# Optimization experiments

Hardware: AMD Instinct MI355X
Metric: run time of the kernel (lower is better)

The kernel has to match this reference:

```python
import jax, jax.numpy as jnp
import numpy as np

B, DIM, H, W = 16, 256, 64, 64
HEADS, DHEAD, MEM = 4, 32, 4
HIDDEN = HEADS * DHEAD


def setup_inputs() -> dict:
    key = jax.random.key(0)
    ks = jax.random.split(key, 4)
    return {
        "x": jax.random.normal(ks[0], (B, DIM, H, W), dtype=jnp.float32),
        "g1": jnp.ones((DIM,), dtype=jnp.float32),
        "w_qkv": jax.random.normal(ks[1], (3 * HIDDEN, DIM), dtype=jnp.float32) * 0.02,
        "mem_kv": jax.random.normal(ks[2], (2, HEADS, DHEAD, MEM), dtype=jnp.float32),
        "w_out": jax.random.normal(ks[3], (DIM, HIDDEN), dtype=jnp.float32) * 0.02,
        "b_out": jnp.zeros((DIM,), dtype=jnp.float32),
        "g2": jnp.ones((DIM,), dtype=jnp.float32),
    }


def _rmsnorm(x, g):
    # F.normalize(x, dim=1) * g * sqrt(dim); g broadcast over (1, dim, 1, 1)
    n = jnp.sqrt(jnp.sum(x * x, axis=1, keepdims=True))
    scale = jnp.asarray(x.shape[1], x.dtype) ** 0.5
    return x / jnp.maximum(n, 1e-12) * g[None, :, None, None] * scale


def reference(x, g1, w_qkv, mem_kv, w_out, b_out, g2):
    b, c, h, w = x.shape
    attn_scale = DHEAD ** -0.5
    xn = _rmsnorm(x, g1)
    # 1x1 conv == channel matmul; chunk(3, dim=1) -> leading axis 3 after reshape
    qkv = jnp.einsum('oc,bchw->bohw', w_qkv, xn)
    qkv = qkv.reshape(b, 3, HEADS, DHEAD, h * w)  # b 3 h d n
    q, k, v = qkv[:, 0], qkv[:, 1], qkv[:, 2]
    mk = jnp.broadcast_to(mem_kv[0][None], (b, HEADS, DHEAD, MEM))
    mv = jnp.broadcast_to(mem_kv[1][None], (b, HEADS, DHEAD, MEM))
    k = jnp.concatenate([mk, k], axis=-1)  # b h d (m+n)
    v = jnp.concatenate([mv, v], axis=-1)
    q = jax.nn.softmax(q, axis=-2) * attn_scale  # softmax over feature dim d
    k = jax.nn.softmax(k, axis=-1)               # softmax over token dim n
    context = jnp.einsum('bhdn,bhen->bhde', k, v)  # d x e per head
    out = jnp.einsum('bhde,bhdn->bhen', context, q)
    out = out.reshape(b, HIDDEN, h, w)
    out = jnp.einsum('oc,bchw->bohw', w_out, out) + b_out[None, :, None, None]
    return _rmsnorm(out, g2)
```

## Files before the change

kernel.cpp:

```cpp
#include <hip/hip_runtime.h>
#include <hip/hip_bf16.h>

#define NB 16
#define DIM 256
#define HW 4096
#define HEADS 4
#define DHEAD 32
#define MEM 4
#define HIDDEN 128

typedef __hip_bfloat16 bf16;
typedef __attribute__((ext_vector_type(8))) short bf16x8;
typedef __attribute__((ext_vector_type(4))) float f32x4;
typedef __attribute__((ext_vector_type(4))) unsigned short us4;

#define AS1 __attribute__((address_space(1)))
#define AS3 __attribute__((address_space(3)))

__device__ __forceinline__ void gld_lds16(const void* g, void* l) {
    __builtin_amdgcn_global_load_lds((const AS1 void*)g, (AS3 void*)l, 16, 0, 0);
}
__device__ __forceinline__ float b2f(short s) {
    union { unsigned int u; float f; } x; x.u = ((unsigned int)(unsigned short)s) << 16; return x.f;
}
__device__ __forceinline__ short f2bs(float f) {
    bf16 h = __float2bfloat16(f);
    return *reinterpret_cast<short*>(&h);
}

constexpr size_t OFF_W1B  = 0;
constexpr size_t OFF_RP   = OFF_W1B + 98304*2;
constexpr size_t OFF_PCTX = OFF_RP + 4*65536*4;
constexpr size_t OFF_CTXN = OFF_PCTX + (size_t)32*64*1056*4;
constexpr size_t OFF_M    = OFF_CTXN + (size_t)64*1024*4;
constexpr size_t OFF_QT   = OFF_M + (size_t)NB*DIM*HIDDEN*2;
constexpr size_t OFF_XT   = OFF_QT + (size_t)NB*HW*HIDDEN*2;

__global__ void k_prep(const float* __restrict__ wqkv, const float* __restrict__ g1,
                       short* __restrict__ w1b) {
    int i = blockIdx.x * 256 + threadIdx.x;
    w1b[i] = f2bs(wqkv[i] * g1[i & (DIM - 1)]);
}

__global__ __launch_bounds__(256) void k_tr(const float* __restrict__ x,
                                            short* __restrict__ xT,
                                            float* __restrict__ rpart) {
    int n0 = blockIdx.x * 64, cy = blockIdx.y, b = blockIdx.z;
    int c0 = cy * 64;
    __shared__ short xs[64 * 65];
    __shared__ float ps[4][64];
    int t = threadIdx.x;
    int ln = t & 63, cb = t >> 6;
    const float* xp = x + ((size_t)b * DIM + c0) * HW + n0;
    float ss = 0.f;
#pragma unroll
    for (int j = 0; j < 16; ++j) {
        int c = cb * 16 + j;
        float v = xp[(size_t)c * HW + ln];
        ss += v * v;
        xs[c * 65 + ln] = f2bs(v);
    }
    ps[cb][ln] = ss;
    __syncthreads();
    if (t < 64)
        rpart[((size_t)cy * NB + b) * HW + n0 + t] = ps[0][t] + ps[1][t] + ps[2][t] + ps[3][t];
    int n = t >> 2, ch = t & 3;
    alignas(16) short tmp[16];
#pragma unroll
    for (int i = 0; i < 16; ++i) tmp[i] = xs[(ch * 16 + i) * 65 + n];
    short* o = xT + ((size_t)b * HW + n0 + n) * DIM + c0 + ch * 16;
    *(bf16x8*)(o)     = *(bf16x8*)(tmp);
    *(bf16x8*)(o + 8) = *(bf16x8*)(tmp + 8);
}

__global__ __launch_bounds__(768) void k_gemm(const short* __restrict__ w1b,
                                              const short* __restrict__ xT,
                                              const float* __restrict__ rpart,
                                              short* __restrict__ qT,
                                              float* __restrict__ pctx) {
    __shared__ __align__(16) char smem[66048];
    float* r2s = (float*)(smem + 65536);
    int nt = blockIdx.x, b = blockIdx.y;
    int t = threadIdx.x;
    int w = t >> 6, lane = t & 63;
    int wr = w >> 1, wc = w & 1;
    int lr = lane & 15, lg = lane >> 4;
    const f32x4 fz = {0.f, 0.f, 0.f, 0.f};
    f32x4 acc[4][4];
#pragma unroll
    for (int m = 0; m < 4; ++m)
#pragma unroll
        for (int n = 0; n < 4; ++n) acc[m][n] = fz;

    if (t < 128) {
        int col = nt * 128 + t;
        float s = rpart[(size_t)b * HW + col] + rpart[(size_t)(16 + b) * HW + col]
                + rpart[(size_t)(32 + b) * HW + col] + rpart[(size_t)(48 + b) * HW + col];
        r2s[t] = 16.0f / fmaxf(sqrtf(s), 1e-12f);
    }

    const short* Bg = xT + ((size_t)b * HW + nt * 128) * 256;
#pragma unroll
    for (int is = 0; is < 5; ++is) {
        int o = is * 12288 + t * 16;
        int row = o >> 9;
        int js = ((o >> 4) & 31) ^ (row & 31);
        gld_lds16(Bg + (size_t)row * 256 + js * 8, smem + o);
    }
    if (t < 256) {
        int o = 61440 + t * 16;
        int row = o >> 9;
        int js = ((o >> 4) & 31) ^ (row & 31);
        gld_lds16(Bg + (size_t)row * 256 + js * 8, smem + o);
    }
    __syncthreads();

    const short* Ag = w1b + (size_t)(wr * 64 + lr) * 256 + lg * 8;
#pragma unroll 2
    for (int kt = 0; kt < 8; ++kt) {
        int kk = kt * 32;
        bf16x8 av[4], bv[4];
#pragma unroll
        for (int m = 0; m < 4; ++m)
            av[m] = *(const bf16x8*)(Ag + (size_t)m * 16 * 256 + kk);
#pragma unroll
        for (int nf = 0; nf < 4; ++nf) {
            int row = wc * 64 + nf * 16 + lr;
            int phys = (kt * 4 + lg) ^ (row & 31);
            bv[nf] = *(const bf16x8*)(smem + row * 512 + phys * 16);
        }
#pragma unroll
        for (int m = 0; m < 4; ++m)
#pragma unroll
            for (int nf = 0; nf < 4; ++nf)
                acc[m][nf] = __builtin_amdgcn_mfma_f32_16x16x32_bf16(av[m], bv[nf], acc[m][nf], 0, 0, 0);
    }

    int gcol0 = nt * 128 + wc * 64 + lr;
    float rv[4];
#pragma unroll
    for (int nf = 0; nf < 4; ++nf) rv[nf] = r2s[wc * 64 + nf * 16 + lr];

    __syncthreads();
    short* ekb = (short*)smem;
    short* vb  = (short*)(smem + 32768);

    if (wr < 2) {
#pragma unroll
        for (int nf = 0; nf < 4; ++nf) {
            int gcol = gcol0 + nf * 16;
#pragma unroll
            for (int a = 0; a < 2; ++a) {
                float v[8];
#pragma unroll
                for (int mm = 0; mm < 2; ++mm)
#pragma unroll
                    for (int q = 0; q < 4; ++q)
                        v[mm * 4 + q] = acc[2 * a + mm][nf][q] * rv[nf];
                float mx = v[0];
#pragma unroll
                for (int i = 1; i < 8; ++i) mx = fmaxf(mx, v[i]);
                mx = fmaxf(mx, __shfl_xor(mx, 16));
                mx = fmaxf(mx, __shfl_xor(mx, 32));
                float sum = 0.f;
#pragma unroll
                for (int i = 0; i < 8; ++i) { v[i] = __expf(v[i] - mx); sum += v[i]; }
                sum += __shfl_xor(sum, 16);
                sum += __shfl_xor(sum, 32);
                float inv = 0.17677669529663689f / sum;
                size_t base = ((size_t)b * HW + gcol) * 128 + (wr * 2 + a) * 32 + lg * 4;
#pragma unroll
                for (int mm = 0; mm < 2; ++mm) {
                    us4 pk;
#pragma unroll
                    for (int q = 0; q < 4; ++q)
                        pk[q] = (unsigned short)f2bs(v[mm * 4 + q] * inv);
                    *(us4*)(qT + base + mm * 16) = pk;
                }
            }
        }
    } else if (wr < 4) {
#pragma unroll
        for (int m = 0; m < 4; ++m)
#pragma unroll
            for (int nf = 0; nf < 4; ++nf)
#pragma unroll
                for (int q = 0; q < 4; ++q) {
                    int rloc = (wr - 2) * 64 + m * 16 + lg * 4 + q;
                    int col = wc * 64 + nf * 16 + lr;
                    int cs = ((((col >> 3) ^ (rloc & 15)) << 3) | (col & 7));
                    ekb[rloc * 128 + cs] = f2bs(__expf(acc[m][nf][q] * rv[nf]));
                }
    } else {
#pragma unroll
        for (int m = 0; m < 4; ++m)
#pragma unroll
            for (int nf = 0; nf < 4; ++nf)
#pragma unroll
                for (int q = 0; q < 4; ++q) {
                    int rloc = (wr - 4) * 64 + m * 16 + lg * 4 + q;
                    int col = wc * 64 + nf * 16 + lr;
                    int cs = ((((col >> 3) ^ (rloc & 15)) << 3) | (col & 7));
                    vb[rloc * 128 + cs] = f2bs(acc[m][nf][q] * rv[nf]);
                }
    }
    __syncthreads();
    if (w < 4) {
        int h = w;
        f32x4 c2[2][2];
        c2[0][0] = fz; c2[0][1] = fz; c2[1][0] = fz; c2[1][1] = fz;
#pragma unroll
        for (int ks = 0; ks < 4; ++ks) {
            int j = ks * 4 + lg;
            bf16x8 a2[2], b2[2];
#pragma unroll
            for (int mm = 0; mm < 2; ++mm) {
                int row = h * 32 + mm * 16 + lr;
                a2[mm] = *(const bf16x8*)(ekb + row * 128 + ((j ^ (row & 15)) << 3));
            }
#pragma unroll
            for (int nn = 0; nn < 2; ++nn) {
                int row = h * 32 + nn * 16 + lr;
                b2[nn] = *(const bf16x8*)(vb + row * 128 + ((j ^ (row & 15)) << 3));
            }
#pragma unroll
            for (int mm = 0; mm < 2; ++mm)
#pragma unroll
                for (int nn = 0; nn < 2; ++nn)
                    c2[mm][nn] = __builtin_amdgcn_mfma_f32_16x16x32_bf16(a2[mm], b2[nn], c2[mm][nn], 0, 0, 0);
        }
        float* o = pctx + ((size_t)nt * 64 + b * 4 + h) * 1056;
#pragma unroll
        for (int mm = 0; mm < 2; ++mm)
#pragma unroll
            for (int nn = 0; nn < 2; ++nn)
#pragma unroll
                for (int qq = 0; qq < 4; ++qq) {
                    int d = mm * 16 + lg * 4 + qq;
                    int e = nn * 16 + lr;
                    o[d * 32 + e] = c2[mm][nn][qq];
                }
    } else if (w >= 8) {
        int hd = (w - 8) * 32 + (lane & 31);
        int half = lane >> 5;
        float rs = 0.f;
#pragma unroll
        for (int blk = 0; blk < 8; ++blk) {
            int chunk = half * 8 + blk;
            bf16x8 e8 = *(const bf16x8*)(ekb + hd * 128 + ((chunk ^ (hd & 15)) << 3));
#pragma unroll
            for (int jj = 0; jj < 8; ++jj) rs += b2f(e8[jj]);
        }
        rs += __shfl_xor(rs, 32);
        if (lane < 32)
            pctx[((size_t)nt * 64 + b * 4 + (w - 8)) * 1056 + 1024 + (lane & 31)] = rs;
    }
}

__global__ __launch_bounds__(256) void k_red(const float* __restrict__ pctx,
                                             const float* __restrict__ memkv,
                                             float* __restrict__ ctxn) {
    int ds = blockIdx.x, bh = blockIdx.y;
    int t = threadIdx.x;
    int dd = t >> 5, ee = t & 31;
    int d = ds * 8 + dd;
    int h = bh & 3;
    __shared__ float rss[8];
    float s = 0.f;
#pragma unroll 8
    for (int c = 0; c < 32; ++c)
        s += pctx[((size_t)c * 64 + bh) * 1056 + d * 32 + ee];
    if (t < 8) {
        int d2 = ds * 8 + t;
        float rs = 0.f;
#pragma unroll 8
        for (int c = 0; c < 32; ++c)
            rs += pctx[((size_t)c * 64 + bh) * 1056 + 1024 + d2];
#pragma unroll
        for (int m2 = 0; m2 < MEM; ++m2) rs += __expf(memkv[(h * 32 + d2) * MEM + m2]);
        rss[t] = rs;
    }
    float mem = 0.f;
#pragma unroll
    for (int m2 = 0; m2 < MEM; ++m2)
        mem += __expf(memkv[(h * 32 + d) * MEM + m2]) * memkv[512 + (h * 32 + ee) * MEM + m2];
    __syncthreads();
    ctxn[(size_t)bh * 1024 + d * 32 + ee] = (s + mem) / rss[dd];
}

__global__ __launch_bounds__(256) void k_M2(const float* __restrict__ ctxn,
                                            const float* __restrict__ wout,
                                            short* __restrict__ Mmat) {
    int og = blockIdx.x, b = blockIdx.y;
    __shared__ float ctx[4 * 33 * 33];
    __shared__ float wsw[32 * 136];
    int t = threadIdx.x;
#pragma unroll
    for (int j = 0; j < 16; ++j) {
        int e = t + j * 256;
        int h = e >> 10, dd = (e >> 5) & 31, ee = e & 31;
        ctx[h * 1089 + dd * 33 + ee] = ctxn[(size_t)(b * 4 + h) * 1024 + (e & 1023)];
    }
#pragma unroll
    for (int j = 0; j < 4; ++j) {
        int e4 = t + j * 256;
        int row = e4 >> 5, c = (e4 & 31) * 4;
        f32x4 w4 = *(const f32x4*)(wout + (size_t)(og * 32 + row) * HIDDEN + c);
        *(f32x4*)(wsw + row * 136 + (c >> 5) * 34 + (c & 31)) = w4;
    }
    __syncthreads();
    int ol = t >> 3, hg = t & 7;
    alignas(16) short out16[16];
#pragma unroll
    for (int ii = 0; ii < 16; ++ii) {
        int hd = hg * 16 + ii;
        int h = hd >> 5, dd = hd & 31;
        float s = 0.f;
#pragma unroll
        for (int e = 0; e < 32; ++e)
            s += wsw[ol * 136 + h * 34 + e] * ctx[h * 1089 + dd * 33 + e];
        out16[ii] = f2bs(s);
    }
    short* op = Mmat + ((size_t)(b * 256 + og * 32 + ol)) * 128 + hg * 16;
    *(bf16x8*)(op)     = *(bf16x8*)(out16);
    *(bf16x8*)(op + 8) = *(bf16x8*)(out16 + 8);
}

__global__ __launch_bounds__(256) void k_out2(const short* __restrict__ Mmat,
                                              const short* __restrict__ qT,
                                              const float* __restrict__ bout,
                                              const float* __restrict__ g2,
                                              float* __restrict__ out) {
    int nt = blockIdx.x, b = blockIdx.y;
    __shared__ short As[256 * 64];
    __shared__ short Bs[64 * 64];
    __shared__ float sw[4][80];
    __shared__ float r2s[64];
    int t = threadIdx.x;
    int wave = t >> 6, lane = t & 63;
    int lr = lane & 15, lg = lane >> 4;
    const short* Ag = Mmat + (size_t)b * 256 * 128;
    const short* Bg = qT + ((size_t)b * HW + nt * 64) * 128;
    const f32x4 fz = {0.f, 0.f, 0.f, 0.f};
    f32x4 acc[4][4];
#pragma unroll
    for (int m = 0; m < 4; ++m)
#pragma unroll
        for (int n = 0; n < 4; ++n) acc[m][n] = fz;

    for (int kk = 0; kk < 128; kk += 64) {
        if (kk) __syncthreads();
#pragma unroll
        for (int is = 0; is < 8; ++is) {
            int o = is * 4096 + t * 16;
            int rr2 = o >> 7;
            int js = ((o >> 4) & 7) ^ (rr2 & 7);
            gld_lds16(Ag + (size_t)rr2 * 128 + kk + js * 8, (char*)As + o);
        }
#pragma unroll
        for (int is = 0; is < 2; ++is) {
            int o = is * 4096 + t * 16;
            int rr2 = o >> 7;
            int js = ((o >> 4) & 7) ^ (rr2 & 7);
            gld_lds16(Bg + (size_t)rr2 * 128 + kk + js * 8, (char*)Bs + o);
        }
        __syncthreads();
#pragma unroll
        for (int ks = 0; ks < 2; ++ks) {
            bf16x8 av[4], bv[4];
            int j = lg + 4 * ks;
#pragma unroll
            for (int m = 0; m < 4; ++m) {
                int row = wave * 64 + m * 16 + lr;
                av[m] = *(const bf16x8*)((const char*)As + row * 128 + ((j ^ (row & 7)) << 4));
            }
#pragma unroll
            for (int n = 0; n < 4; ++n) {
                int row = n * 16 + lr;
                bv[n] = *(const bf16x8*)((const char*)Bs + row * 128 + ((j ^ (row & 7)) << 4));
            }
#pragma unroll
            for (int m = 0; m < 4; ++m)
#pragma unroll
                for (int n = 0; n < 4; ++n)
                    acc[m][n] = __builtin_amdgcn_mfma_f32_16x16x32_bf16(av[m], bv[n], acc[m][n], 0, 0, 0);
        }
    }
    float bb[4][4], gg[4][4];
#pragma unroll
    for (int m = 0; m < 4; ++m)
#pragma unroll
        for (int q = 0; q < 4; ++q) {
            int row = wave * 64 + m * 16 + lg * 4 + q;
            bb[m][q] = bout[row];
            gg[m][q] = g2[row];
        }
    float ssn[4] = {0.f, 0.f, 0.f, 0.f};
#pragma unroll
    for (int n = 0; n < 4; ++n)
#pragma unroll
        for (int m = 0; m < 4; ++m)
#pragma unroll
            for (int q = 0; q < 4; ++q) {
                float val = acc[m][n][q] + bb[m][q];
                acc[m][n][q] = val;
                ssn[n] += val * val;
            }
#pragma unroll
    for (int n = 0; n < 4; ++n) {
        ssn[n] += __shfl_xor(ssn[n], 16);
        ssn[n] += __shfl_xor(ssn[n], 32);
    }
    if (lg == 0) {
#pragma unroll
        for (int n = 0; n < 4; ++n) sw[wave][n * 16 + lr] = ssn[n];
    }
    __syncthreads();
    if (t < 64) {
        float s = sw[0][t] + sw[1][t] + sw[2][t] + sw[3][t];
        r2s[t] = 16.0f / fmaxf(sqrtf(s), 1e-12f);
    }
    __syncthreads();
    float* op = out + (size_t)b * DIM * HW + nt * 64;
#pragma unroll
    for (int n = 0; n < 4; ++n) {
        float rc = r2s[n * 16 + lr];
#pragma unroll
        for (int m = 0; m < 4; ++m)
#pragma unroll
            for (int q = 0; q < 4; ++q) {
                int row = wave * 64 + m * 16 + lg * 4 + q;
                op[(size_t)row * HW + n * 16 + lr] = acc[m][n][q] * rc * gg[m][q];
            }
    }
}

extern "C" void kernel_launch(void* const* d_in, const int* in_sizes, int n_in,
                              void* d_out, int out_size, void* d_ws, size_t ws_size,
                              hipStream_t stream) {
    const float* x     = (const float*)d_in[0];
    const float* g1    = (const float*)d_in[1];
    const float* wqkv  = (const float*)d_in[2];
    const float* memkv = (const float*)d_in[3];
    const float* wout  = (const float*)d_in[4];
    const float* bout  = (const float*)d_in[5];
    const float* g2    = (const float*)d_in[6];
    float* out = (float*)d_out;
    char* ws = (char*)d_ws;

    short* w1b  = (short*)(ws + OFF_W1B);
    float* rpart= (float*)(ws + OFF_RP);
    float* pctx = (float*)(ws + OFF_PCTX);
    float* ctxn = (float*)(ws + OFF_CTXN);
    short* Mmat = (short*)(ws + OFF_M);
    short* qT   = (short*)(ws + OFF_QT);
    short* xT   = (short*)(ws + OFF_XT);

    k_prep<<<384, 256, 0, stream>>>(wqkv, g1, w1b);
    k_tr<<<dim3(64, 4, NB), 256, 0, stream>>>(x, xT, rpart);
    k_gemm<<<dim3(32, NB), 768, 0, stream>>>(w1b, xT, rpart, qT, pctx);
    k_red<<<dim3(4, 64), 256, 0, stream>>>(pctx, memkv, ctxn);
    k_M2<<<dim3(8, NB), 256, 0, stream>>>(ctxn, wout, Mmat);
    k_out2<<<dim3(64, NB), 256, 0, stream>>>(Mmat, qT, bout, g2, out);
}
```

Measured before the change: 91.56 us.

## Halve QKV GEMM token tile to 64 with 384-thread blocks and register A prefetch

The fused QKV projection and context kernel now processes 64 tokens per block with 6 waves instead of 128 tokens with 12 waves. That doubles the grid to 1024 blocks and halves LDS use so up to three blocks can reside per CU. Each wave holds its full 64-row weight slice in registers, loaded in two halves, rather than reloading per k-step. The softmax-K and V staging in LDS drops the XOR swizzle. The partial-context buffer and the reduction kernel double to 64 chunks, which adds reduction traffic and raises register pressure.

```diff
diff --git a/kernel.cpp b/kernel.cpp
--- a/kernel.cpp
+++ b/kernel.cpp
@@ -31,7 +31,7 @@
 constexpr size_t OFF_W1B  = 0;
 constexpr size_t OFF_RP   = OFF_W1B + 98304*2;
 constexpr size_t OFF_PCTX = OFF_RP + 4*65536*4;
-constexpr size_t OFF_CTXN = OFF_PCTX + (size_t)32*64*1056*4;
+constexpr size_t OFF_CTXN = OFF_PCTX + (size_t)64*64*1056*4;
 constexpr size_t OFF_M    = OFF_CTXN + (size_t)64*1024*4;
 constexpr size_t OFF_QT   = OFF_M + (size_t)NB*DIM*HIDDEN*2;
 constexpr size_t OFF_XT   = OFF_QT + (size_t)NB*HW*HIDDEN*2;
@@ -73,17 +73,17 @@
     *(bf16x8*)(o + 8) = *(bf16x8*)(tmp + 8);
 }
 
-__global__ __launch_bounds__(768) void k_gemm(const short* __restrict__ w1b,
-                                              const short* __restrict__ xT,
-                                              const float* __restrict__ rpart,
-                                              short* __restrict__ qT,
-                                              float* __restrict__ pctx) {
-    __shared__ __align__(16) char smem[66048];
-    float* r2s = (float*)(smem + 65536);
+__global__ __launch_bounds__(384, 3) void k_gemm(const short* __restrict__ w1b,
+                                                 const short* __restrict__ xT,
+                                                 const float* __restrict__ rpart,
+                                                 short* __restrict__ qT,
+                                                 float* __restrict__ pctx) {
+    __shared__ __align__(16) char smem[33280];
+    float* r2s = (float*)(smem + 32768);
     int nt = blockIdx.x, b = blockIdx.y;
+    int n0g = nt * 64;
     int t = threadIdx.x;
     int w = t >> 6, lane = t & 63;
-    int wr = w >> 1, wc = w & 1;
     int lr = lane & 15, lg = lane >> 4;
     const f32x4 fz = {0.f, 0.f, 0.f, 0.f};
     f32x4 acc[4][4];
@@ -92,63 +92,84 @@
 #pragma unroll
         for (int n = 0; n < 4; ++n) acc[m][n] = fz;
 
+    const short* Bg = xT + ((size_t)b * HW + n0g) * 256;
+#pragma unroll
+    for (int is = 0; is < 5; ++is) {
+        int o = is * 6144 + t * 16;
+        int row = o >> 9;
+        int js = ((o >> 4) & 31) ^ (row & 31);
+        gld_lds16(Bg + (size_t)row * 256 + js * 8, smem + o);
+    }
     if (t < 128) {
-        int col = nt * 128 + t;
+        int o = 30720 + t * 16;
+        int row = o >> 9;
+        int js = ((o >> 4) & 31) ^ (row & 31);
+        gld_lds16(Bg + (size_t)row * 256 + js * 8, smem + o);
+    }
+    if (t < 64) {
+        int col = n0g + t;
         float s = rpart[(size_t)b * HW + col] + rpart[(size_t)(16 + b) * HW + col]
                 + rpart[(size_t)(32 + b) * HW + col] + rpart[(size_t)(48 + b) * HW + col];
         r2s[t] = 16.0f / fmaxf(sqrtf(s), 1e-12f);
     }
-
-    const short* Bg = xT + ((size_t)b * HW + nt * 128) * 256;
-#pragma unroll
-    for (int is = 0; is < 5; ++is) {
-        int o = is * 12288 + t * 16;
-        int row = o >> 9;
-        int js = ((o >> 4) & 31) ^ (row & 31);
-        gld_lds16(Bg + (size_t)row * 256 + js * 8, smem + o);
-    }
-    if (t < 256) {
-        int o = 61440 + t * 16;
-        int row = o >> 9;
-        int js = ((o >> 4) & 31) ^ (row & 31);
-        gld_lds16(Bg + (size_t)row * 256 + js * 8, smem + o);
-    }
-    __syncthreads();
-
-    const short* Ag = w1b + (size_t)(wr * 64 + lr) * 256 + lg * 8;
-#pragma unroll 2
-    for (int kt = 0; kt < 8; ++kt) {
-        int kk = kt * 32;
-        bf16x8 av[4], bv[4];
-#pragma unroll
-        for (int m = 0; m < 4; ++m)
-            av[m] = *(const bf16x8*)(Ag + (size_t)m * 16 * 256 + kk);
+    const short* Ag = w1b + (size_t)(w * 64 + lr) * 256 + lg * 8;
+    bf16x8 a1[4][4];
+#pragma unroll
+    for (int m = 0; m < 4; ++m)
+#pragma unroll
+        for (int kc = 0; kc < 4; ++kc)
+            a1[m][kc] = *(const bf16x8*)(Ag + (size_t)m * 16 * 256 + kc * 32);
+    __syncthreads();
+
+#pragma unroll
+    for (int kc = 0; kc < 4; ++kc) {
+        bf16x8 bv[4];
 #pragma unroll
         for (int nf = 0; nf < 4; ++nf) {
-            int row = wc * 64 + nf * 16 + lr;
-            int phys = (kt * 4 + lg) ^ (row & 31);
+            int row = nf * 16 + lr;
+            int phys = (kc * 4 + lg) ^ (row & 31);
             bv[nf] = *(const bf16x8*)(smem + row * 512 + phys * 16);
         }
 #pragma unroll
         for (int m = 0; m < 4; ++m)
 #pragma unroll
             for (int nf = 0; nf < 4; ++nf)
-                acc[m][nf] = __builtin_amdgcn_mfma_f32_16x16x32_bf16(av[m], bv[nf], acc[m][nf], 0, 0, 0);
-    }
-
-    int gcol0 = nt * 128 + wc * 64 + lr;
+                acc[m][nf] = __builtin_amdgcn_mfma_f32_16x16x32_bf16(a1[m][kc], bv[nf], acc[m][nf], 0, 0, 0);
+    }
+    bf16x8 a2[4][4];
+#pragma unroll
+    for (int m = 0; m < 4; ++m)
+#pragma unroll
+        for (int kc = 0; kc < 4; ++kc)
+            a2[m][kc] = *(const bf16x8*)(Ag + (size_t)m * 16 * 256 + 128 + kc * 32);
+#pragma unroll
+    for (int kc = 0; kc < 4; ++kc) {
+        bf16x8 bv[4];
+#pragma unroll
+        for (int nf = 0; nf < 4; ++nf) {
+            int row = nf * 16 + lr;
+            int phys = ((kc + 4) * 4 + lg) ^ (row & 31);
+            bv[nf] = *(const bf16x8*)(smem + row * 512 + phys * 16);
+        }
+#pragma unroll
+        for (int m = 0; m < 4; ++m)
+#pragma unroll
+            for (int nf = 0; nf < 4; ++nf)
+                acc[m][nf] = __builtin_amdgcn_mfma_f32_16x16x32_bf16(a2[m][kc], bv[nf], acc[m][nf], 0, 0, 0);
+    }
+
     float rv[4];
 #pragma unroll
-    for (int nf = 0; nf < 4; ++nf) rv[nf] = r2s[wc * 64 + nf * 16 + lr];
+    for (int nf = 0; nf < 4; ++nf) rv[nf] = r2s[nf * 16 + lr];
 
     __syncthreads();
     short* ekb = (short*)smem;
-    short* vb  = (short*)(smem + 32768);
-
-    if (wr < 2) {
+    short* vb  = (short*)(smem + 16384);
+
+    if (w < 2) {
 #pragma unroll
         for (int nf = 0; nf < 4; ++nf) {
-            int gcol = gcol0 + nf * 16;
+            int gcol = n0g + nf * 16 + lr;
 #pragma unroll
             for (int a = 0; a < 2; ++a) {
                 float v[8];
@@ -168,7 +189,7 @@
                 sum += __shfl_xor(sum, 16);
                 sum += __shfl_xor(sum, 32);
                 float inv = 0.17677669529663689f / sum;
-                size_t base = ((size_t)b * HW + gcol) * 128 + (wr * 2 + a) * 32 + lg * 4;
+                size_t base = ((size_t)b * HW + gcol) * 128 + (w * 2 + a) * 32 + lg * 4;
 #pragma unroll
                 for (int mm = 0; mm < 2; ++mm) {
                     us4 pk;
@@ -179,17 +200,15 @@
                 }
             }
         }
-    } else if (wr < 4) {
+    } else if (w < 4) {
 #pragma unroll
         for (int m = 0; m < 4; ++m)
 #pragma unroll
             for (int nf = 0; nf < 4; ++nf)
 #pragma unroll
                 for (int q = 0; q < 4; ++q) {
-                    int rloc = (wr - 2) * 64 + m * 16 + lg * 4 + q;
-                    int col = wc * 64 + nf * 16 + lr;
-                    int cs = ((((col >> 3) ^ (rloc & 15)) << 3) | (col & 7));
-                    ekb[rloc * 128 + cs] = f2bs(__expf(acc[m][nf][q] * rv[nf]));
+                    int rloc = (w - 2) * 64 + m * 16 + lg * 4 + q;
+                    ekb[rloc * 64 + nf * 16 + lr] = f2bs(__expf(acc[m][nf][q] * rv[nf]));
                 }
     } else {
 #pragma unroll
@@ -198,10 +217,8 @@
             for (int nf = 0; nf < 4; ++nf)
 #pragma unroll
                 for (int q = 0; q < 4; ++q) {
-                    int rloc = (wr - 4) * 64 + m * 16 + lg * 4 + q;
-                    int col = wc * 64 + nf * 16 + lr;
-                    int cs = ((((col >> 3) ^ (rloc & 15)) << 3) | (col & 7));
-                    vb[rloc * 128 + cs] = f2bs(acc[m][nf][q] * rv[nf]);
+                    int rloc = (w - 4) * 64 + m * 16 + lg * 4 + q;
+                    vb[rloc * 64 + nf * 16 + lr] = f2bs(acc[m][nf][q] * rv[nf]);
                 }
     }
     __syncthreads();
@@ -210,24 +227,20 @@
         f32x4 c2[2][2];
         c2[0][0] = fz; c2[0][1] = fz; c2[1][0] = fz; c2[1][1] = fz;
 #pragma unroll
-        for (int ks = 0; ks < 4; ++ks) {
-            int j = ks * 4 + lg;
-            bf16x8 a2[2], b2[2];
-#pragma unroll
-            for (int mm = 0; mm < 2; ++mm) {
-                int row = h * 32 + mm * 16 + lr;
-                a2[mm] = *(const bf16x8*)(ekb + row * 128 + ((j ^ (row & 15)) << 3));
-            }
-#pragma unroll
-            for (int nn = 0; nn < 2; ++nn) {
-                int row = h * 32 + nn * 16 + lr;
-                b2[nn] = *(const bf16x8*)(vb + row * 128 + ((j ^ (row & 15)) << 3));
-            }
+        for (int ks = 0; ks < 2; ++ks) {
+            int j = lg + 4 * ks;
+            bf16x8 a2b[2], b2[2];
 #pragma unroll
             for (int mm = 0; mm < 2; ++mm)
+                a2b[mm] = *(const bf16x8*)(ekb + (h * 32 + mm * 16 + lr) * 64 + j * 8);
+#pragma unroll
+            for (int nn = 0; nn < 2; ++nn)
+                b2[nn] = *(const bf16x8*)(vb + (h * 32 + nn * 16 + lr) * 64 + j * 8);
+#pragma unroll
+            for (int mm = 0; mm < 2; ++mm)
 #pragma unroll
                 for (int nn = 0; nn < 2; ++nn)
-                    c2[mm][nn] = __builtin_amdgcn_mfma_f32_16x16x32_bf16(a2[mm], b2[nn], c2[mm][nn], 0, 0, 0);
+                    c2[mm][nn] = __builtin_amdgcn_mfma_f32_16x16x32_bf16(a2b[mm], b2[nn], c2[mm][nn], 0, 0, 0);
         }
         float* o = pctx + ((size_t)nt * 64 + b * 4 + h) * 1056;
 #pragma unroll
@@ -240,20 +253,16 @@
                     int e = nn * 16 + lr;
                     o[d * 32 + e] = c2[mm][nn][qq];
                 }
-    } else if (w >= 8) {
-        int hd = (w - 8) * 32 + (lane & 31);
-        int half = lane >> 5;
+    } else {
+        int hd = (w - 4) * 64 + lane;
         float rs = 0.f;
 #pragma unroll
         for (int blk = 0; blk < 8; ++blk) {
-            int chunk = half * 8 + blk;
-            bf16x8 e8 = *(const bf16x8*)(ekb + hd * 128 + ((chunk ^ (hd & 15)) << 3));
-#pragma unroll
-            for (int jj = 0; jj < 8; ++jj) rs += b2f(e8[jj]);
-        }
-        rs += __shfl_xor(rs, 32);
-        if (lane < 32)
-            pctx[((size_t)nt * 64 + b * 4 + (w - 8)) * 1056 + 1024 + (lane & 31)] = rs;
+            bf16x8 e8 = *(const bf16x8*)(ekb + hd * 64 + blk * 8);
+#pragma unroll
+            for (int j = 0; j < 8; ++j) rs += b2f(e8[j]);
+        }
+        pctx[((size_t)nt * 64 + b * 4 + (hd >> 5)) * 1056 + 1024 + (hd & 31)] = rs;
     }
 }
 
@@ -268,13 +277,13 @@
     __shared__ float rss[8];
     float s = 0.f;
 #pragma unroll 8
-    for (int c = 0; c < 32; ++c)
+    for (int c = 0; c < 64; ++c)
         s += pctx[((size_t)c * 64 + bh) * 1056 + d * 32 + ee];
     if (t < 8) {
         int d2 = ds * 8 + t;
         float rs = 0.f;
 #pragma unroll 8
-        for (int c = 0; c < 32; ++c)
+        for (int c = 0; c < 64; ++c)
             rs += pctx[((size_t)c * 64 + bh) * 1056 + 1024 + d2];
 #pragma unroll
         for (int m2 = 0; m2 < MEM; ++m2) rs += __expf(memkv[(h * 32 + d2) * MEM + m2]);
@@ -458,7 +467,7 @@
 
     k_prep<<<384, 256, 0, stream>>>(wqkv, g1, w1b);
     k_tr<<<dim3(64, 4, NB), 256, 0, stream>>>(x, xT, rpart);
-    k_gemm<<<dim3(32, NB), 768, 0, stream>>>(w1b, xT, rpart, qT, pctx);
+    k_gemm<<<dim3(64, NB), 384, 0, stream>>>(w1b, xT, rpart, qT, pctx);
     k_red<<<dim3(4, 64), 256, 0, stream>>>(pctx, memkv, ctxn);
     k_M2<<<dim3(8, NB), 256, 0, stream>>>(ctxn, wout, Mmat);
     k_out2<<<dim3(64, NB), 256, 0, stream>>>(Mmat, qT, bout, g2, out);
```

New measurement: 102.0 us. 11.4% more time.
